# Kernel tuning notes

Hardware: AMD Instinct MI355X
Metric: run time of the kernel (lower is better)

Reference implementation:

```python
import jax, jax.numpy as jnp
import numpy as np

D_MODEL = 1024
N_HEADS = 16
DEPTH = D_MODEL // N_HEADS
DFF = 4096
B, S = 2, 2048
EPS = 1e-6


def layer_norm(x, gamma, beta):
    m = jnp.mean(x, axis=-1, keepdims=True)
    v = jnp.mean(jnp.square(x - m), axis=-1, keepdims=True)
    return (x - m) * jax.lax.rsqrt(v + EPS) * gamma + beta


def setup_inputs() -> dict:
    key = jax.random.key(0)
    ks = jax.random.split(key, 16)
    s = 0.02
    x = jax.random.normal(ks[0], (B, S, D_MODEL), dtype=jnp.float32)
    # causal mask: 1.0 where attention is NOT allowed (upper triangle)
    mask = (1.0 - jnp.tril(jnp.ones((S, S), dtype=jnp.float32)))[None, None, :, :]
    return {
        "x": x,
        "mask": mask,
        "wq": jax.random.normal(ks[1], (D_MODEL, D_MODEL), jnp.float32) * s,
        "bq": jnp.zeros((D_MODEL,), jnp.float32),
        "wk": jax.random.normal(ks[2], (D_MODEL, D_MODEL), jnp.float32) * s,
        "bk": jnp.zeros((D_MODEL,), jnp.float32),
        "wv": jax.random.normal(ks[3], (D_MODEL, D_MODEL), jnp.float32) * s,
        "bv": jnp.zeros((D_MODEL,), jnp.float32),
        "wo": jax.random.normal(ks[4], (D_MODEL, D_MODEL), jnp.float32) * s,
        "bo": jnp.zeros((D_MODEL,), jnp.float32),
        "g1": jnp.ones((D_MODEL,), jnp.float32),
        "be1": jnp.zeros((D_MODEL,), jnp.float32),
        "w1": jax.random.normal(ks[5], (D_MODEL, DFF), jnp.float32) * s,
        "b1": jnp.zeros((DFF,), jnp.float32),
        "w2": jax.random.normal(ks[6], (DFF, D_MODEL), jnp.float32) * s,
        "b2": jnp.zeros((D_MODEL,), jnp.float32),
        "g2": jnp.ones((D_MODEL,), jnp.float32),
        "be2": jnp.zeros((D_MODEL,), jnp.float32),
    }


def reference(x, mask, wq, bq, wk, bk, wv, bv, wo, bo, g1, be1, w1, b1, w2, b2, g2, be2):
    b, s = x.shape[0], x.shape[1]

    def heads(t):  # [B,S,D_MODEL] -> [B,H,S,depth]
        return t.reshape(b, s, N_HEADS, DEPTH).transpose(0, 2, 1, 3)

    q = heads(x @ wq + bq)
    k = heads(x @ wk + bk)
    v = heads(x @ wv + bv)

    # [B,H,S,S] scores, materialized as in the original
    logits = jnp.einsum("bhqd,bhkd->bhqk", q, k) / jnp.sqrt(jnp.float32(DEPTH))
    logits = logits + mask * (-1e9)
    attn = jax.nn.softmax(logits, axis=-1)
    ctx = jnp.einsum("bhqk,bhkd->bhqd", attn, v)
    ctx = ctx.transpose(0, 2, 1, 3).reshape(b, s, D_MODEL)
    attn_out = ctx @ wo + bo

    out1 = layer_norm(x + attn_out, g1, be1)
    ffn = jax.nn.relu(out1 @ w1 + b1) @ w2 + b2
    out2 = layer_norm(out1 + ffn, g2, be2)
    return out2  # dropout inactive (training=False)
```

## Files before the change

### kernel.cpp

```cpp
#include <hip/hip_runtime.h>
#include <stdint.h>

typedef unsigned short u16;
typedef unsigned int u32;
typedef __attribute__((ext_vector_type(8))) short short8;
typedef __attribute__((ext_vector_type(4))) float f32x4;

#define NHEADS 16
#define SEQ 2048
#define DM 1024
#define MROWS 4096
#define FF 4096

static_assert(sizeof(short8) == 16, "short8 must be 16B");

__device__ __forceinline__ u16 f2b(float f) {
  u32 u = __float_as_uint(f);
  u += 0x7fffu + ((u >> 16) & 1u);
  return (u16)(u >> 16);
}
__device__ __forceinline__ u32 f2b2(float lo, float hi) {
  u32 a = __float_as_uint(lo); a += 0x7fffu + ((a >> 16) & 1u);
  u32 b = __float_as_uint(hi); b += 0x7fffu + ((b >> 16) & 1u);
  return (a >> 16) | (b & 0xffff0000u);
}
__device__ __forceinline__ float b2f(u16 h) { return __uint_as_float(((u32)h) << 16); }

__device__ __forceinline__ void async_cp16(const u16* g, u16* l) {
  __builtin_amdgcn_global_load_lds((const __attribute__((address_space(1))) void*)g,
                                   (__attribute__((address_space(3))) void*)l, 16, 0, 0);
}

__global__ __launch_bounds__(256) void cvt_bf16(const float* __restrict__ in,
                                                u16* __restrict__ out, const int n4) {
  const int i = blockIdx.x * 256 + threadIdx.x;
  if (i < n4) {
    const float4 v = ((const float4*)in)[i];
    uint2 o; o.x = f2b2(v.x, v.y); o.y = f2b2(v.z, v.w);
    ((uint2*)out)[i] = o;
  }
}

template <typename TIN>
__global__ __launch_bounds__(256) void transpose_bf16(const TIN* __restrict__ in,
                                                      u16* __restrict__ out, const int K,
                                                      const int N, const long isz, const long osz) {
  __shared__ float tile[32][33];
  const TIN* inz = in + (long)blockIdx.z * isz;
  u16* outz = out + (long)blockIdx.z * osz;
  const int n0 = blockIdx.x * 32, k0 = blockIdx.y * 32;
  const int tx = threadIdx.x & 31, ty = threadIdx.x >> 5;
#pragma unroll
  for (int i = 0; i < 4; i++) {
    const int r = ty + i * 8;
    float val;
    if constexpr (sizeof(TIN) == 4) { val = inz[(long)(k0 + r) * N + n0 + tx]; }
    else { val = b2f(inz[(long)(k0 + r) * N + n0 + tx]); }
    tile[r][tx] = val;
  }
  __syncthreads();
#pragma unroll
  for (int i = 0; i < 4; i++) {
    const int r = ty + i * 8;
    outz[(long)(n0 + r) * K + k0 + tx] = f2b(tile[tx][r]);
  }
}

#define BM 128
#define BN 128
#define BK 64
#define EPI_QKV 0
#define EPI_RELUB 2
#define EPI_PART 3

template <int EPI>
__global__ __launch_bounds__(256, 2) void gemm_bt(
    const u16* __restrict__ A, const u16* __restrict__ Bt, const int M, const int N,
    const int KITER, const int LDA, const int KOFF,
    const float* __restrict__ bias0, const float* __restrict__ bias1,
    const float* __restrict__ bias2,
    float* __restrict__ outF, u16* __restrict__ outB, u16* __restrict__ outQ,
    u16* __restrict__ outK, u16* __restrict__ outV) {
  __shared__ u16 As[BM * BK];
  __shared__ u16 Bs[BN * BK];
  const int tid = threadIdx.x;
  const int lane = tid & 63;
  const int wv = tid >> 6;
  const int quad = lane >> 4;
  const int lm = lane & 15;
  const int tn = blockIdx.x * BN;
  const int tm = blockIdx.y * BM;
  const int wr = (wv >> 1) * 64;
  const int wc = (wv & 1) * 64;
  const int wslotbase = tid & ~63;
  const long zoff = (long)blockIdx.z * KOFF;
  const u16* Ap = A + zoff;
  const u16* Btp = Bt + zoff;

  const f32x4 z4 = {0.f, 0.f, 0.f, 0.f};
  f32x4 acc[4][4];
#pragma unroll
  for (int i = 0; i < 4; i++)
#pragma unroll
    for (int j = 0; j < 4; j++) acc[i][j] = z4;

  for (int kk = 0; kk < KITER; kk += BK) {
    __syncthreads();
#pragma unroll
    for (int t = 0; t < 4; t++) {
      const int slot = t * 256 + tid;
      const int row = slot >> 3;
      const int c = (slot & 7) ^ (row & 7);
      async_cp16(Ap + (long)(tm + row) * LDA + kk + c * 8,
                 As + (long)(t * 256 + wslotbase) * 8);
    }
#pragma unroll
    for (int t = 0; t < 4; t++) {
      const int slot = t * 256 + tid;
      const int row = slot >> 3;
      const int c = (slot & 7) ^ (row & 7);
      async_cp16(Btp + (long)(tn + row) * LDA + kk + c * 8,
                 Bs + (long)(t * 256 + wslotbase) * 8);
    }
    __syncthreads();
#pragma unroll
    for (int ks = 0; ks < 2; ks++) {
      short8 af[4], bf[4];
#pragma unroll
      for (int mi = 0; mi < 4; mi++) {
        const int row = wr + mi * 16 + lm;
        const int cc = (4 * ks + quad) ^ (row & 7);
        af[mi] = *(const short8*)(As + row * 64 + cc * 8);
      }
#pragma unroll
      for (int ni = 0; ni < 4; ni++) {
        const int row = wc + ni * 16 + lm;
        const int cc = (4 * ks + quad) ^ (row & 7);
        bf[ni] = *(const short8*)(Bs + row * 64 + cc * 8);
      }
#pragma unroll
      for (int mi = 0; mi < 4; mi++)
#pragma unroll
        for (int ni = 0; ni < 4; ni++)
          acc[mi][ni] =
              __builtin_amdgcn_mfma_f32_16x16x32_bf16(af[mi], bf[ni], acc[mi][ni], 0, 0, 0);
    }
  }

  if constexpr (EPI == EPI_QKV) {
    const int which = tn >> 10;
    const float* bs = which == 0 ? bias0 : (which == 1 ? bias1 : bias2);
    u16* os = which == 0 ? outQ : (which == 1 ? outK : outV);
    const float scale = which == 0 ? 0.125f * 1.44269504f : 1.0f;
#pragma unroll
    for (int ni = 0; ni < 4; ni++) {
      const int n = tn + wc + ni * 16 + lm;
      const int hd = n & 1023;
      const int h = hd >> 6, dep = hd & 63;
      const float bval = bs[hd];
#pragma unroll
      for (int mi = 0; mi < 4; mi++) {
#pragma unroll
        for (int r = 0; r < 4; r++) {
          const int m = tm + wr + mi * 16 + quad * 4 + r;
          const int bb = m >> 11, ss = m & 2047;
          os[(((long)(bb * NHEADS + h) * SEQ + ss) << 6) + dep] =
              f2b((acc[mi][ni][r] + bval) * scale);
        }
      }
    }
  } else if constexpr (EPI == EPI_PART) {
    float* po = outF + (long)blockIdx.z * M * N;
#pragma unroll
    for (int mi = 0; mi < 4; mi++) {
#pragma unroll
      for (int r = 0; r < 4; r++) {
        const int m = tm + wr + mi * 16 + quad * 4 + r;
        const long rowo = (long)m * N;
#pragma unroll
        for (int ni = 0; ni < 4; ni++) {
          const int n = tn + wc + ni * 16 + lm;
          po[rowo + n] = acc[mi][ni][r];
        }
      }
    }
  } else {
#pragma unroll
    for (int mi = 0; mi < 4; mi++) {
#pragma unroll
      for (int r = 0; r < 4; r++) {
        const int m = tm + wr + mi * 16 + quad * 4 + r;
        const long rowo = (long)m * N;
#pragma unroll
        for (int ni = 0; ni < 4; ni++) {
          const int n = tn + wc + ni * 16 + lm;
          const float v = acc[mi][ni][r] + bias0[n];
          outB[rowo + n] = f2b(fmaxf(v, 0.f));
        }
      }
    }
  }
}

__global__ __launch_bounds__(256, 2) void attn_fused(const u16* __restrict__ Q,
                                                     const u16* __restrict__ K,
                                                     const u16* __restrict__ Vt,
                                                     u16* __restrict__ O) {
  __shared__ u16 Ks[2][64 * 64];
  __shared__ u16 Vs[2][64 * 64];
  __shared__ u16 Ps[4][32 * 72];
  const int tid = threadIdx.x;
  const int lane = tid & 63, w = tid >> 6, quad = lane >> 4, lm = lane & 15;
  const int bid = blockIdx.x;
  const int idx = bid >> 5;
  const int hb = bid & 31;
  const int h = hb & 15, b = hb >> 4;
  const int j = (idx < 8) ? idx : (23 - idx);
  const int myqt = (w < 2) ? (31 - j) : j;
  const int rbase = myqt * 64 + (w & 1) * 32;
  const int nk = 32 - j;
  const long bh = (long)(b * NHEADS + h);
  const u16* Qb = Q + bh * SEQ * 64;
  const u16* Kb = K + bh * SEQ * 64;
  const u16* Vb = Vt + bh * (long)64 * SEQ;
  const int wslot = tid & ~63;

  short8 qf[2][2];
#pragma unroll
  for (int mi = 0; mi < 2; mi++)
#pragma unroll
    for (int ks = 0; ks < 2; ks++)
      qf[mi][ks] = *(const short8*)(Qb + (long)(rbase + mi * 16 + lm) * 64 + ks * 32 + quad * 8);

  const f32x4 z4 = {0.f, 0.f, 0.f, 0.f};
  f32x4 ctx[2][4];
#pragma unroll
  for (int mi = 0; mi < 2; mi++)
#pragma unroll
    for (int d = 0; d < 4; d++) ctx[mi][d] = z4;
  float lacc[2] = {0.f, 0.f};
  u16* myP = (u16*)Ps[w];

#pragma unroll
  for (int i = 0; i < 2; i++) {
    const int slot = i * 256 + tid;
    const int row = slot >> 3;
    const int cg = (slot & 7) ^ (row & 7);
    async_cp16(Kb + (long)row * 64 + cg * 8, Ks[0] + (i * 256 + wslot) * 8);
    async_cp16(Vb + (long)row * SEQ + cg * 8, Vs[0] + (i * 256 + wslot) * 8);
  }

  for (int kt = 0; kt < nk; kt++) {
    const int cur = kt & 1;
    const int k0 = kt * 64;
    __syncthreads();
    if (kt + 1 < nk) {
      const int kn = k0 + 64;
#pragma unroll
      for (int i = 0; i < 2; i++) {
        const int slot = i * 256 + tid;
        const int row = slot >> 3;
        const int cg = (slot & 7) ^ (row & 7);
        async_cp16(Kb + (long)(kn + row) * 64 + cg * 8, Ks[1 - cur] + (i * 256 + wslot) * 8);
        async_cp16(Vb + (long)row * SEQ + kn + cg * 8, Vs[1 - cur] + (i * 256 + wslot) * 8);
      }
    }
    if (k0 < rbase + 32) {
      const u16* Kc = Ks[cur];
      const u16* Vc = Vs[cur];
      short8 kf[4][2];
#pragma unroll
      for (int ni = 0; ni < 4; ni++) {
        const int row = ni * 16 + lm;
        const int r8 = row & 7;
#pragma unroll
        for (int ks = 0; ks < 2; ks++) {
          const int cc = (ks * 4 + quad) ^ r8;
          kf[ni][ks] = *(const short8*)(Kc + row * 64 + cc * 8);
        }
      }
      short8 vf[2][4];
#pragma unroll
      for (int kc = 0; kc < 2; kc++)
#pragma unroll
        for (int dni = 0; dni < 4; dni++) {
          const int row = dni * 16 + lm;
          const int cc = (kc * 4 + quad) ^ (row & 7);
          vf[kc][dni] = *(const short8*)(Vc + row * 64 + cc * 8);
        }
#pragma unroll
      for (int mi = 0; mi < 2; mi++) {
        const int rmin = rbase + mi * 16;
        if (k0 < rmin + 16) {
          f32x4 sa[4];
#pragma unroll
          for (int i = 0; i < 4; i++) sa[i] = z4;
#pragma unroll
          for (int ks = 0; ks < 2; ks++)
#pragma unroll
            for (int ni = 0; ni < 4; ni++)
              sa[ni] = __builtin_amdgcn_mfma_f32_16x16x32_bf16(kf[ni][ks], qf[mi][ks],
                                                               sa[ni], 0, 0, 0);
          const int qrow = rmin + lm;
          if (k0 + 63 > rmin) {
#pragma unroll
            for (int ni = 0; ni < 4; ni++)
#pragma unroll
              for (int r = 0; r < 4; r++)
                if (k0 + ni * 16 + quad * 4 + r > qrow) sa[ni][r] = -1e9f;
          }
          float tsum = 0.f;
#pragma unroll
          for (int ni = 0; ni < 4; ni++) {
            const float p0 = exp2f(sa[ni][0]);
            const float p1 = exp2f(sa[ni][1]);
            const float p2 = exp2f(sa[ni][2]);
            const float p3 = exp2f(sa[ni][3]);
            tsum += (p0 + p1) + (p2 + p3);
            uint2 o; o.x = f2b2(p0, p1); o.y = f2b2(p2, p3);
            *(uint2*)(myP + (mi * 16 + lm) * 72 + ni * 16 + quad * 4) = o;
          }
          lacc[mi] += tsum;
#pragma unroll
          for (int kc = 0; kc < 2; kc++) {
            const short8 bp = *(const short8*)(myP + (mi * 16 + lm) * 72 + kc * 32 + quad * 8);
#pragma unroll
            for (int dni = 0; dni < 4; dni++)
              ctx[mi][dni] =
                  __builtin_amdgcn_mfma_f32_16x16x32_bf16(vf[kc][dni], bp, ctx[mi][dni], 0, 0, 0);
          }
        }
      }
    }
  }
#pragma unroll
  for (int mi = 0; mi < 2; mi++) {
    float l = lacc[mi];
    l += __shfl_xor(l, 16);
    l += __shfl_xor(l, 32);
    const float inv = 1.0f / l;
    const int s = rbase + mi * 16 + lm;
    const long base = (long)(b * SEQ + s) * DM + h * 64;
#pragma unroll
    for (int dni = 0; dni < 4; dni++) {
      uint2 o;
      o.x = f2b2(ctx[mi][dni][0] * inv, ctx[mi][dni][1] * inv);
      o.y = f2b2(ctx[mi][dni][2] * inv, ctx[mi][dni][3] * inv);
      *(uint2*)(O + base + dni * 16 + quad * 4) = o;
    }
  }
}

template <bool WB>
__global__ __launch_bounds__(256) void layernorm2_k(const float* __restrict__ p0,
                                                    const float* __restrict__ p1,
                                                    const float* __restrict__ resid,
                                                    const float* __restrict__ bias,
                                                    const float* __restrict__ gam,
                                                    const float* __restrict__ bet,
                                                    float* __restrict__ outF,
                                                    u16* __restrict__ outB) {
  __shared__ float red[8];
  const int row = blockIdx.x, tid = threadIdx.x;
  const long off = (long)row * DM;
  const float4 a4 = ((const float4*)(p0 + off))[tid];
  const float4 b4v = ((const float4*)(p1 + off))[tid];
  const float4 r4 = ((const float4*)(resid + off))[tid];
  const float4 bi4 = ((const float4*)bias)[tid];
  float4 v;
  v.x = a4.x + b4v.x + r4.x + bi4.x;
  v.y = a4.y + b4v.y + r4.y + bi4.y;
  v.z = a4.z + b4v.z + r4.z + bi4.z;
  v.w = a4.w + b4v.w + r4.w + bi4.w;
  float s = v.x + v.y + v.z + v.w;
  s += __shfl_xor(s, 1); s += __shfl_xor(s, 2); s += __shfl_xor(s, 4);
  s += __shfl_xor(s, 8); s += __shfl_xor(s, 16); s += __shfl_xor(s, 32);
  if ((tid & 63) == 0) red[tid >> 6] = s;
  __syncthreads();
  const float mean = (red[0] + red[1] + red[2] + red[3]) * (1.f / DM);
  const float dx = v.x - mean, dy = v.y - mean, dz = v.z - mean, dw = v.w - mean;
  float q = dx * dx + dy * dy + dz * dz + dw * dw;
  q += __shfl_xor(q, 1); q += __shfl_xor(q, 2); q += __shfl_xor(q, 4);
  q += __shfl_xor(q, 8); q += __shfl_xor(q, 16); q += __shfl_xor(q, 32);
  if ((tid & 63) == 0) red[4 + (tid >> 6)] = q;
  __syncthreads();
  const float var = (red[4] + red[5] + red[6] + red[7]) * (1.f / DM);
  const float rs = rsqrtf(var + 1e-6f);
  const float4 g4 = ((const float4*)gam)[tid];
  const float4 be4 = ((const float4*)bet)[tid];
  const float o0 = dx * rs * g4.x + be4.x;
  const float o1 = dy * rs * g4.y + be4.y;
  const float o2 = dz * rs * g4.z + be4.z;
  const float o3 = dw * rs * g4.w + be4.w;
  ((float4*)(outF + off))[tid] = make_float4(o0, o1, o2, o3);
  if constexpr (WB) {
    uint2 o; o.x = f2b2(o0, o1); o.y = f2b2(o2, o3);
    ((uint2*)(outB + off))[tid] = o;
  }
}

extern "C" void kernel_launch(void* const* d_in, const int* in_sizes, int n_in,
                              void* d_out, int out_size, void* d_ws, size_t ws_size,
                              hipStream_t stream) {
  (void)in_sizes; (void)n_in; (void)out_size; (void)ws_size;
  const float* x = (const float*)d_in[0];
  const float* wq = (const float*)d_in[2];
  const float* bq = (const float*)d_in[3];
  const float* wk = (const float*)d_in[4];
  const float* bk = (const float*)d_in[5];
  const float* wv = (const float*)d_in[6];
  const float* bv = (const float*)d_in[7];
  const float* wo = (const float*)d_in[8];
  const float* bo = (const float*)d_in[9];
  const float* g1 = (const float*)d_in[10];
  const float* be1 = (const float*)d_in[11];
  const float* w1 = (const float*)d_in[12];
  const float* b1 = (const float*)d_in[13];
  const float* w2 = (const float*)d_in[14];
  const float* b2 = (const float*)d_in[15];
  const float* g2 = (const float*)d_in[16];
  const float* be2 = (const float*)d_in[17];
  float* out = (float*)d_out;
  uint8_t* ws = (uint8_t*)d_ws;
  const size_t MB = 1024ull * 1024ull;
  u16* wot = (u16*)(ws + 0 * MB);
  u16* w1t = (u16*)(ws + 2 * MB);
  u16* w2t = (u16*)(ws + 10 * MB);
  u16* btq = (u16*)(ws + 18 * MB);
  u16* xb  = (u16*)(ws + 24 * MB);
  u16* qb  = (u16*)(ws + 32 * MB);
  u16* kb  = (u16*)(ws + 40 * MB);
  u16* vb  = (u16*)(ws + 48 * MB);
  u16* vt  = (u16*)(ws + 56 * MB);
  u16* ctxb = (u16*)(ws + 64 * MB);
  float* part = (float*)(ws + 72 * MB);
  u16* o1b = (u16*)(ws + 104 * MB);
  float* o1f = (float*)(ws + 112 * MB);
  u16* h1 = (u16*)(ws + 18 * MB);

  cvt_bf16<<<dim3(4096), dim3(256), 0, stream>>>(x, xb, (MROWS * DM) / 4);
  transpose_bf16<float><<<dim3(32, 32, 1), dim3(256), 0, stream>>>(wq, btq, 1024, 1024, 0, 0);
  transpose_bf16<float><<<dim3(32, 32, 1), dim3(256), 0, stream>>>(wk, btq + 1024 * 1024, 1024, 1024, 0, 0);
  transpose_bf16<float><<<dim3(32, 32, 1), dim3(256), 0, stream>>>(wv, btq + 2 * 1024 * 1024, 1024, 1024, 0, 0);
  transpose_bf16<float><<<dim3(32, 32, 1), dim3(256), 0, stream>>>(wo, wot, 1024, 1024, 0, 0);
  transpose_bf16<float><<<dim3(128, 32, 1), dim3(256), 0, stream>>>(w1, w1t, 1024, 4096, 0, 0);
  transpose_bf16<float><<<dim3(32, 128, 1), dim3(256), 0, stream>>>(w2, w2t, 4096, 1024, 0, 0);

  gemm_bt<EPI_QKV><<<dim3(24, 32), dim3(256), 0, stream>>>(
      xb, btq, MROWS, 3072, 1024, 1024, 0, bq, bk, bv, nullptr, nullptr, qb, kb, vb);

  transpose_bf16<u16><<<dim3(2, 64, 32), dim3(256), 0, stream>>>(
      vb, vt, 2048, 64, (long)2048 * 64, (long)64 * 2048);

  attn_fused<<<dim3(512), dim3(256), 0, stream>>>(qb, kb, vt, ctxb);

  gemm_bt<EPI_PART><<<dim3(8, 32, 2), dim3(256), 0, stream>>>(
      ctxb, wot, MROWS, 1024, 512, 1024, 512, nullptr, nullptr, nullptr, part, nullptr,
      nullptr, nullptr, nullptr);

  layernorm2_k<true><<<dim3(4096), dim3(256), 0, stream>>>(
      part, part + (long)MROWS * DM, x, bo, g1, be1, o1f, o1b);

  gemm_bt<EPI_RELUB><<<dim3(32, 32), dim3(256), 0, stream>>>(
      o1b, w1t, MROWS, 4096, 1024, 1024, 0, b1, nullptr, nullptr, nullptr, h1, nullptr,
      nullptr, nullptr);

  gemm_bt<EPI_PART><<<dim3(8, 32, 2), dim3(256), 0, stream>>>(
      h1, w2t, MROWS, 1024, 2048, 4096, 2048, nullptr, nullptr, nullptr, part, nullptr,
      nullptr, nullptr, nullptr);

  layernorm2_k<false><<<dim3(4096), dim3(256), 0, stream>>>(
      part, part + (long)MROWS * DM, o1f, b2, g2, be2, out, nullptr);
}
```

Measured before the change: 375.5 us.

## Split-KV attention with combine kernel, fuse prep kernels, single-pass layernorm stats

Attention is repartitioned so each block handles one 64-row query tile with 16 rows per wave. For the long upper-half tiles the key range is split into two halves, whose partial contexts and row sums go to a workspace and are merged by a new combine kernel. This is meant to balance the causal work and raise occupancy (launch bounds 3) at the cost of extra partial writes and one more launch. The seven weight and input conversion launches are merged into one kernel, and layernorm now computes sum and sum of squares in one reduction, which saves a barrier but is less numerically robust.

```diff
diff --git a/kernel.cpp b/kernel.cpp
--- a/kernel.cpp
+++ b/kernel.cpp
@@ -31,13 +31,52 @@
                                    (__attribute__((address_space(3))) void*)l, 16, 0, 0);
 }
 
-__global__ __launch_bounds__(256) void cvt_bf16(const float* __restrict__ in,
-                                                u16* __restrict__ out, const int n4) {
-  const int i = blockIdx.x * 256 + threadIdx.x;
-  if (i < n4) {
-    const float4 v = ((const float4*)in)[i];
+__global__ __launch_bounds__(256) void prep_k(const float* __restrict__ x,
+                                              const float* __restrict__ wq,
+                                              const float* __restrict__ wk,
+                                              const float* __restrict__ wv,
+                                              const float* __restrict__ wo,
+                                              const float* __restrict__ w1,
+                                              const float* __restrict__ w2,
+                                              u16* __restrict__ xb, u16* __restrict__ btq,
+                                              u16* __restrict__ wot, u16* __restrict__ w1t,
+                                              u16* __restrict__ w2t) {
+  const int bid = blockIdx.x, tid = threadIdx.x;
+  if (bid < 4096) {
+    const int i = bid * 256 + tid;
+    const float4 v = ((const float4*)x)[i];
     uint2 o; o.x = f2b2(v.x, v.y); o.y = f2b2(v.z, v.w);
-    ((uint2*)out)[i] = o;
+    ((uint2*)xb)[i] = o;
+    return;
+  }
+  __shared__ float tile[32][33];
+  const int tb = bid - 4096;
+  const float* in; u16* out; int N, K, n0, k0;
+  if (tb < 4096) {
+    const int m = tb >> 10, t = tb & 1023;
+    if (m == 0) { in = wq; out = btq; }
+    else if (m == 1) { in = wk; out = btq + 1024 * 1024; }
+    else if (m == 2) { in = wv; out = btq + 2 * 1024 * 1024; }
+    else { in = wo; out = wot; }
+    N = 1024; K = 1024; n0 = (t & 31) * 32; k0 = (t >> 5) * 32;
+  } else if (tb < 8192) {
+    const int t = tb - 4096;
+    in = w1; out = w1t; N = 4096; K = 1024; n0 = (t & 127) * 32; k0 = (t >> 7) * 32;
+  } else {
+    const int t = tb - 8192;
+    in = w2; out = w2t; N = 1024; K = 4096; n0 = (t & 31) * 32; k0 = (t >> 5) * 32;
+  }
+  const int tx = tid & 31, ty = tid >> 5;
+#pragma unroll
+  for (int i = 0; i < 4; i++) {
+    const int r = ty + i * 8;
+    tile[r][tx] = in[(long)(k0 + r) * N + n0 + tx];
+  }
+  __syncthreads();
+#pragma unroll
+  for (int i = 0; i < 4; i++) {
+    const int r = ty + i * 8;
+    out[(long)(n0 + r) * K + k0 + tx] = f2b(tile[tx][r]);
   }
 }
 
@@ -202,59 +241,66 @@
   }
 }
 
-__global__ __launch_bounds__(256, 2) void attn_fused(const u16* __restrict__ Q,
+__global__ __launch_bounds__(256, 3) void attn_fused(const u16* __restrict__ Q,
                                                      const u16* __restrict__ K,
                                                      const u16* __restrict__ Vt,
-                                                     u16* __restrict__ O) {
+                                                     u16* __restrict__ O,
+                                                     float* __restrict__ part,
+                                                     float* __restrict__ lpart) {
   __shared__ u16 Ks[2][64 * 64];
   __shared__ u16 Vs[2][64 * 64];
-  __shared__ u16 Ps[4][32 * 72];
+  __shared__ u16 Ps[4][16 * 72];
   const int tid = threadIdx.x;
   const int lane = tid & 63, w = tid >> 6, quad = lane >> 4, lm = lane & 15;
   const int bid = blockIdx.x;
-  const int idx = bid >> 5;
-  const int hb = bid & 31;
+  const int idx = bid >> 5, hb = bid & 31;
   const int h = hb & 15, b = hb >> 4;
-  const int j = (idx < 8) ? idx : (23 - idx);
-  const int myqt = (w < 2) ? (31 - j) : j;
-  const int rbase = myqt * 64 + (w & 1) * 32;
-  const int nk = 32 - j;
+  int qt, c0, nkl, half;
+  if (idx < 32) {
+    qt = 16 + (idx >> 1);
+    const int nk = qt + 1;
+    const int h0 = (nk + 1) >> 1;
+    half = idx & 1;
+    if (half == 0) { c0 = 0; nkl = h0; } else { c0 = h0; nkl = nk - h0; }
+  } else {
+    qt = 47 - idx; c0 = 0; nkl = qt + 1; half = -1;
+  }
   const long bh = (long)(b * NHEADS + h);
   const u16* Qb = Q + bh * SEQ * 64;
   const u16* Kb = K + bh * SEQ * 64;
   const u16* Vb = Vt + bh * (long)64 * SEQ;
+  const int rbase = qt * 64 + w * 16;
   const int wslot = tid & ~63;
 
-  short8 qf[2][2];
-#pragma unroll
-  for (int mi = 0; mi < 2; mi++)
-#pragma unroll
-    for (int ks = 0; ks < 2; ks++)
-      qf[mi][ks] = *(const short8*)(Qb + (long)(rbase + mi * 16 + lm) * 64 + ks * 32 + quad * 8);
+  short8 qf[2];
+#pragma unroll
+  for (int ks = 0; ks < 2; ks++)
+    qf[ks] = *(const short8*)(Qb + (long)(rbase + lm) * 64 + ks * 32 + quad * 8);
 
   const f32x4 z4 = {0.f, 0.f, 0.f, 0.f};
-  f32x4 ctx[2][4];
-#pragma unroll
-  for (int mi = 0; mi < 2; mi++)
-#pragma unroll
-    for (int d = 0; d < 4; d++) ctx[mi][d] = z4;
-  float lacc[2] = {0.f, 0.f};
+  f32x4 ctx[4];
+#pragma unroll
+  for (int d = 0; d < 4; d++) ctx[d] = z4;
+  float lacc = 0.f;
   u16* myP = (u16*)Ps[w];
 
-#pragma unroll
-  for (int i = 0; i < 2; i++) {
-    const int slot = i * 256 + tid;
-    const int row = slot >> 3;
-    const int cg = (slot & 7) ^ (row & 7);
-    async_cp16(Kb + (long)row * 64 + cg * 8, Ks[0] + (i * 256 + wslot) * 8);
-    async_cp16(Vb + (long)row * SEQ + cg * 8, Vs[0] + (i * 256 + wslot) * 8);
-  }
-
-  for (int kt = 0; kt < nk; kt++) {
-    const int cur = kt & 1;
-    const int k0 = kt * 64;
+  {
+    const int k0p = c0 * 64;
+#pragma unroll
+    for (int i = 0; i < 2; i++) {
+      const int slot = i * 256 + tid;
+      const int row = slot >> 3;
+      const int cg = (slot & 7) ^ (row & 7);
+      async_cp16(Kb + (long)(k0p + row) * 64 + cg * 8, Ks[0] + (i * 256 + wslot) * 8);
+      async_cp16(Vb + (long)row * SEQ + k0p + cg * 8, Vs[0] + (i * 256 + wslot) * 8);
+    }
+  }
+
+  for (int t = 0; t < nkl; t++) {
+    const int cur = t & 1;
+    const int k0 = (c0 + t) * 64;
     __syncthreads();
-    if (kt + 1 < nk) {
+    if (t + 1 < nkl) {
       const int kn = k0 + 64;
 #pragma unroll
       for (int i = 0; i < 2; i++) {
@@ -265,90 +311,109 @@
         async_cp16(Vb + (long)row * SEQ + kn + cg * 8, Vs[1 - cur] + (i * 256 + wslot) * 8);
       }
     }
-    if (k0 < rbase + 32) {
-      const u16* Kc = Ks[cur];
-      const u16* Vc = Vs[cur];
-      short8 kf[4][2];
-#pragma unroll
-      for (int ni = 0; ni < 4; ni++) {
-        const int row = ni * 16 + lm;
-        const int r8 = row & 7;
-#pragma unroll
-        for (int ks = 0; ks < 2; ks++) {
-          const int cc = (ks * 4 + quad) ^ r8;
-          kf[ni][ks] = *(const short8*)(Kc + row * 64 + cc * 8);
-        }
-      }
-      short8 vf[2][4];
-#pragma unroll
-      for (int kc = 0; kc < 2; kc++)
-#pragma unroll
-        for (int dni = 0; dni < 4; dni++) {
-          const int row = dni * 16 + lm;
-          const int cc = (kc * 4 + quad) ^ (row & 7);
-          vf[kc][dni] = *(const short8*)(Vc + row * 64 + cc * 8);
-        }
-#pragma unroll
-      for (int mi = 0; mi < 2; mi++) {
-        const int rmin = rbase + mi * 16;
-        if (k0 < rmin + 16) {
-          f32x4 sa[4];
-#pragma unroll
-          for (int i = 0; i < 4; i++) sa[i] = z4;
-#pragma unroll
-          for (int ks = 0; ks < 2; ks++)
-#pragma unroll
-            for (int ni = 0; ni < 4; ni++)
-              sa[ni] = __builtin_amdgcn_mfma_f32_16x16x32_bf16(kf[ni][ks], qf[mi][ks],
-                                                               sa[ni], 0, 0, 0);
-          const int qrow = rmin + lm;
-          if (k0 + 63 > rmin) {
-#pragma unroll
-            for (int ni = 0; ni < 4; ni++)
-#pragma unroll
-              for (int r = 0; r < 4; r++)
-                if (k0 + ni * 16 + quad * 4 + r > qrow) sa[ni][r] = -1e9f;
-          }
-          float tsum = 0.f;
-#pragma unroll
-          for (int ni = 0; ni < 4; ni++) {
-            const float p0 = exp2f(sa[ni][0]);
-            const float p1 = exp2f(sa[ni][1]);
-            const float p2 = exp2f(sa[ni][2]);
-            const float p3 = exp2f(sa[ni][3]);
-            tsum += (p0 + p1) + (p2 + p3);
-            uint2 o; o.x = f2b2(p0, p1); o.y = f2b2(p2, p3);
-            *(uint2*)(myP + (mi * 16 + lm) * 72 + ni * 16 + quad * 4) = o;
-          }
-          lacc[mi] += tsum;
-#pragma unroll
-          for (int kc = 0; kc < 2; kc++) {
-            const short8 bp = *(const short8*)(myP + (mi * 16 + lm) * 72 + kc * 32 + quad * 8);
-#pragma unroll
-            for (int dni = 0; dni < 4; dni++)
-              ctx[mi][dni] =
-                  __builtin_amdgcn_mfma_f32_16x16x32_bf16(vf[kc][dni], bp, ctx[mi][dni], 0, 0, 0);
-          }
-        }
-      }
-    }
-  }
-#pragma unroll
-  for (int mi = 0; mi < 2; mi++) {
-    float l = lacc[mi];
-    l += __shfl_xor(l, 16);
-    l += __shfl_xor(l, 32);
+    const u16* Kc = Ks[cur];
+    const u16* Vc = Vs[cur];
+    short8 kf[4][2];
+#pragma unroll
+    for (int ni = 0; ni < 4; ni++) {
+      const int row = ni * 16 + lm;
+      const int r8 = row & 7;
+#pragma unroll
+      for (int ks = 0; ks < 2; ks++) {
+        const int cc = (ks * 4 + quad) ^ r8;
+        kf[ni][ks] = *(const short8*)(Kc + row * 64 + cc * 8);
+      }
+    }
+    f32x4 sa[4];
+#pragma unroll
+    for (int i = 0; i < 4; i++) sa[i] = z4;
+#pragma unroll
+    for (int ks = 0; ks < 2; ks++)
+#pragma unroll
+      for (int ni = 0; ni < 4; ni++)
+        sa[ni] = __builtin_amdgcn_mfma_f32_16x16x32_bf16(kf[ni][ks], qf[ks], sa[ni], 0, 0, 0);
+    const int qrow = rbase + lm;
+    if (k0 + 63 > rbase) {
+#pragma unroll
+      for (int ni = 0; ni < 4; ni++)
+#pragma unroll
+        for (int r = 0; r < 4; r++)
+          if (k0 + ni * 16 + quad * 4 + r > qrow) sa[ni][r] = -1e9f;
+    }
+    float tsum = 0.f;
+#pragma unroll
+    for (int ni = 0; ni < 4; ni++) {
+      const float p0 = exp2f(sa[ni][0]);
+      const float p1 = exp2f(sa[ni][1]);
+      const float p2 = exp2f(sa[ni][2]);
+      const float p3 = exp2f(sa[ni][3]);
+      tsum += (p0 + p1) + (p2 + p3);
+      uint2 o; o.x = f2b2(p0, p1); o.y = f2b2(p2, p3);
+      *(uint2*)(myP + lm * 72 + ni * 16 + quad * 4) = o;
+    }
+    lacc += tsum;
+#pragma unroll
+    for (int kc = 0; kc < 2; kc++) {
+      const short8 bp = *(const short8*)(myP + lm * 72 + kc * 32 + quad * 8);
+#pragma unroll
+      for (int dni = 0; dni < 4; dni++) {
+        const int row = dni * 16 + lm;
+        const int cc = (kc * 4 + quad) ^ (row & 7);
+        const short8 vfr = *(const short8*)(Vc + row * 64 + cc * 8);
+        ctx[dni] = __builtin_amdgcn_mfma_f32_16x16x32_bf16(vfr, bp, ctx[dni], 0, 0, 0);
+      }
+    }
+  }
+  float l = lacc;
+  l += __shfl_xor(l, 16);
+  l += __shfl_xor(l, 32);
+  if (half < 0) {
     const float inv = 1.0f / l;
-    const int s = rbase + mi * 16 + lm;
+    const int s = rbase + lm;
     const long base = (long)(b * SEQ + s) * DM + h * 64;
 #pragma unroll
     for (int dni = 0; dni < 4; dni++) {
       uint2 o;
-      o.x = f2b2(ctx[mi][dni][0] * inv, ctx[mi][dni][1] * inv);
-      o.y = f2b2(ctx[mi][dni][2] * inv, ctx[mi][dni][3] * inv);
+      o.x = f2b2(ctx[dni][0] * inv, ctx[dni][1] * inv);
+      o.y = f2b2(ctx[dni][2] * inv, ctx[dni][3] * inv);
       *(uint2*)(O + base + dni * 16 + quad * 4) = o;
     }
-  }
+  } else {
+    const long pt = ((long)(hb * 16 + (qt - 16))) * 2 + half;
+    float* po = part + pt * 4096 + (w * 16 + lm) * 64;
+#pragma unroll
+    for (int dni = 0; dni < 4; dni++)
+      *(float4*)(po + dni * 16 + quad * 4) =
+          make_float4(ctx[dni][0], ctx[dni][1], ctx[dni][2], ctx[dni][3]);
+    if (quad == 0) lpart[pt * 64 + w * 16 + lm] = l;
+  }
+}
+
+__global__ __launch_bounds__(256) void attn_combine(const float* __restrict__ part,
+                                                    const float* __restrict__ lpart,
+                                                    u16* __restrict__ O) {
+  const int g = blockIdx.x;
+  const int hb = g >> 4, qtr = g & 15;
+  const int h = hb & 15, b = hb >> 4;
+  const int qt = 16 + qtr;
+  const long pt0 = ((long)(hb * 16 + qtr)) * 2;
+  const float* p0 = part + pt0 * 4096;
+  const float* p1 = p0 + 4096;
+  const float* lp = lpart + pt0 * 64;
+  const int tid = threadIdx.x;
+  const int row = tid >> 2, d0 = (tid & 3) * 16;
+  const float inv = 1.0f / (lp[row] + lp[64 + row]);
+  const long off = (long)(b * SEQ + qt * 64 + row) * DM + h * 64 + d0;
+  u32 o[8];
+#pragma unroll
+  for (int i = 0; i < 4; i++) {
+    const float4 a = *(const float4*)(p0 + row * 64 + d0 + i * 4);
+    const float4 c = *(const float4*)(p1 + row * 64 + d0 + i * 4);
+    o[i * 2 + 0] = f2b2((a.x + c.x) * inv, (a.y + c.y) * inv);
+    o[i * 2 + 1] = f2b2((a.z + c.z) * inv, (a.w + c.w) * inv);
+  }
+  *(uint4*)(O + off) = make_uint4(o[0], o[1], o[2], o[3]);
+  *(uint4*)(O + off + 8) = make_uint4(o[4], o[5], o[6], o[7]);
 }
 
 template <bool WB>
@@ -372,26 +437,26 @@
   v.y = a4.y + b4v.y + r4.y + bi4.y;
   v.z = a4.z + b4v.z + r4.z + bi4.z;
   v.w = a4.w + b4v.w + r4.w + bi4.w;
-  float s = v.x + v.y + v.z + v.w;
-  s += __shfl_xor(s, 1); s += __shfl_xor(s, 2); s += __shfl_xor(s, 4);
-  s += __shfl_xor(s, 8); s += __shfl_xor(s, 16); s += __shfl_xor(s, 32);
-  if ((tid & 63) == 0) red[tid >> 6] = s;
+  float s1 = v.x + v.y + v.z + v.w;
+  float s2 = v.x * v.x + v.y * v.y + v.z * v.z + v.w * v.w;
+  s1 += __shfl_xor(s1, 1); s2 += __shfl_xor(s2, 1);
+  s1 += __shfl_xor(s1, 2); s2 += __shfl_xor(s2, 2);
+  s1 += __shfl_xor(s1, 4); s2 += __shfl_xor(s2, 4);
+  s1 += __shfl_xor(s1, 8); s2 += __shfl_xor(s2, 8);
+  s1 += __shfl_xor(s1, 16); s2 += __shfl_xor(s2, 16);
+  s1 += __shfl_xor(s1, 32); s2 += __shfl_xor(s2, 32);
+  if ((tid & 63) == 0) { red[tid >> 6] = s1; red[4 + (tid >> 6)] = s2; }
   __syncthreads();
   const float mean = (red[0] + red[1] + red[2] + red[3]) * (1.f / DM);
-  const float dx = v.x - mean, dy = v.y - mean, dz = v.z - mean, dw = v.w - mean;
-  float q = dx * dx + dy * dy + dz * dz + dw * dw;
-  q += __shfl_xor(q, 1); q += __shfl_xor(q, 2); q += __shfl_xor(q, 4);
-  q += __shfl_xor(q, 8); q += __shfl_xor(q, 16); q += __shfl_xor(q, 32);
-  if ((tid & 63) == 0) red[4 + (tid >> 6)] = q;
-  __syncthreads();
-  const float var = (red[4] + red[5] + red[6] + red[7]) * (1.f / DM);
+  const float ex2 = (red[4] + red[5] + red[6] + red[7]) * (1.f / DM);
+  const float var = fmaxf(ex2 - mean * mean, 0.f);
   const float rs = rsqrtf(var + 1e-6f);
   const float4 g4 = ((const float4*)gam)[tid];
   const float4 be4 = ((const float4*)bet)[tid];
-  const float o0 = dx * rs * g4.x + be4.x;
-  const float o1 = dy * rs * g4.y + be4.y;
-  const float o2 = dz * rs * g4.z + be4.z;
-  const float o3 = dw * rs * g4.w + be4.w;
+  const float o0 = (v.x - mean) * rs * g4.x + be4.x;
+  const float o1 = (v.y - mean) * rs * g4.y + be4.y;
+  const float o2 = (v.z - mean) * rs * g4.z + be4.z;
+  const float o3 = (v.w - mean) * rs * g4.w + be4.w;
   ((float4*)(outF + off))[tid] = make_float4(o0, o1, o2, o3);
   if constexpr (WB) {
     uint2 o; o.x = f2b2(o0, o1); o.y = f2b2(o2, o3);
@@ -434,17 +499,14 @@
   u16* vt  = (u16*)(ws + 56 * MB);
   u16* ctxb = (u16*)(ws + 64 * MB);
   float* part = (float*)(ws + 72 * MB);
+  float* apart = (float*)(ws + 72 * MB);
+  float* lpart = (float*)(ws + 89 * MB);
   u16* o1b = (u16*)(ws + 104 * MB);
   float* o1f = (float*)(ws + 112 * MB);
   u16* h1 = (u16*)(ws + 18 * MB);
 
-  cvt_bf16<<<dim3(4096), dim3(256), 0, stream>>>(x, xb, (MROWS * DM) / 4);
-  transpose_bf16<float><<<dim3(32, 32, 1), dim3(256), 0, stream>>>(wq, btq, 1024, 1024, 0, 0);
-  transpose_bf16<float><<<dim3(32, 32, 1), dim3(256), 0, stream>>>(wk, btq + 1024 * 1024, 1024, 1024, 0, 0);
-  transpose_bf16<float><<<dim3(32, 32, 1), dim3(256), 0, stream>>>(wv, btq + 2 * 1024 * 1024, 1024, 1024, 0, 0);
-  transpose_bf16<float><<<dim3(32, 32, 1), dim3(256), 0, stream>>>(wo, wot, 1024, 1024, 0, 0);
-  transpose_bf16<float><<<dim3(128, 32, 1), dim3(256), 0, stream>>>(w1, w1t, 1024, 4096, 0, 0);
-  transpose_bf16<float><<<dim3(32, 128, 1), dim3(256), 0, stream>>>(w2, w2t, 4096, 1024, 0, 0);
+  prep_k<<<dim3(16384), dim3(256), 0, stream>>>(x, wq, wk, wv, wo, w1, w2, xb, btq, wot,
+                                                w1t, w2t);
 
   gemm_bt<EPI_QKV><<<dim3(24, 32), dim3(256), 0, stream>>>(
       xb, btq, MROWS, 3072, 1024, 1024, 0, bq, bk, bv, nullptr, nullptr, qb, kb, vb);
@@ -452,7 +514,8 @@
   transpose_bf16<u16><<<dim3(2, 64, 32), dim3(256), 0, stream>>>(
       vb, vt, 2048, 64, (long)2048 * 64, (long)64 * 2048);
 
-  attn_fused<<<dim3(512), dim3(256), 0, stream>>>(qb, kb, vt, ctxb);
+  attn_fused<<<dim3(1536), dim3(256), 0, stream>>>(qb, kb, vt, ctxb, apart, lpart);
+  attn_combine<<<dim3(512), dim3(256), 0, stream>>>(apart, lpart, ctxb);
 
   gemm_bt<EPI_PART><<<dim3(8, 32, 2), dim3(256), 0, stream>>>(
       ctxb, wot, MROWS, 1024, 512, 1024, 512, nullptr, nullptr, nullptr, part, nullptr,
```

Result: faster. 357.7 us (-4.8%).
